# Optimization experiments

Measured on AMD Instinct MI355X. Metric: run time of the kernel, lower is better.

Reference implementation:

```python
import jax, jax.numpy as jnp
import numpy as np

NUM_EXPERTS = 8
TOP_K = 2
AUX_COEF = 0.01
B, S, D, H = 4, 2048, 1024, 684


def setup_inputs() -> dict:
    key = jax.random.key(0)
    ks = jax.random.split(key, 5)
    scale_d = 1.0 / np.sqrt(D)
    scale_h = 1.0 / np.sqrt(H)
    return {
        "x": jax.random.normal(ks[0], (B, S, D), dtype=jnp.float32),
        "router_w": jax.random.normal(ks[1], (NUM_EXPERTS, D), dtype=jnp.float32) * scale_d,
        "w1": jax.random.normal(ks[2], (NUM_EXPERTS, H, D), dtype=jnp.float32) * scale_d,
        "w2": jax.random.normal(ks[3], (NUM_EXPERTS, D, H), dtype=jnp.float32) * scale_h,
        "w3": jax.random.normal(ks[4], (NUM_EXPERTS, H, D), dtype=jnp.float32) * scale_d,
    }


def reference(x, router_w, w1, w2, w3):
    b, s, d = x.shape
    xf = x.reshape(-1, d)                                   # [T, d]
    probs = jax.nn.softmax(xf @ router_w.T, axis=-1)        # [T, E]
    topk_probs, topk_idx = jax.lax.top_k(probs, TOP_K)      # [T, k]

    # aux load-balancing loss (uses top-1 assignment density)
    density = jnp.mean(jax.nn.one_hot(topk_idx[:, 0], NUM_EXPERTS, dtype=xf.dtype), axis=0)
    aux_loss = AUX_COEF * jnp.sum(density * probs.mean(axis=0)) * NUM_EXPERTS

    # per-token per-expert combine weight (sums probs if an expert repeats across slots)
    combine = jnp.sum(jax.nn.one_hot(topk_idx, NUM_EXPERTS, dtype=xf.dtype)
                      * topk_probs[..., None], axis=1)      # [T, E]

    out = jnp.zeros_like(xf)
    for e in range(NUM_EXPERTS):  # fixed small expert loop
        h = jax.nn.silu(xf @ w1[e].T) * (xf @ w3[e].T)      # [T, H] SwiGLU
        out = out + combine[:, e:e + 1] * (h @ w2[e].T)     # weighted scatter-combine
    return out.reshape(b, s, d), aux_loss
```

## Files before the change

kernel.cpp:

```cpp
#include <hip/hip_runtime.h>
#include <hip/hip_bf16.h>

#define T_TOK 8192
#define DMODEL 1024
#define HDIM 684
#define HPAD 704
#define NEXP 8

typedef short  bf16x8  __attribute__((ext_vector_type(8)));
typedef float  f32x4   __attribute__((ext_vector_type(4)));

__device__ inline unsigned short f2bu(float f) {
    __hip_bfloat16 h = __float2bfloat16(f);
    return *reinterpret_cast<unsigned short*>(&h);
}

typedef const __attribute__((address_space(1))) unsigned int* gas_p;
typedef __attribute__((address_space(3))) unsigned int* las_p;
__device__ inline void ld_lds16(const unsigned short* g, unsigned short* l) {
    __builtin_amdgcn_global_load_lds((gas_p)g, (las_p)l, 16, 0, 0);
}


__global__ __launch_bounds__(256) void cvt_bf16x4(
    const float* __restrict__ src, unsigned short* __restrict__ dst, int n4)
{
    int i = blockIdx.x * 256 + threadIdx.x;
    if (i >= n4) return;
    float4 v = ((const float4*)src)[i];
    ushort4 o = make_ushort4(f2bu(v.x), f2bu(v.y), f2bu(v.z), f2bu(v.w));
    ((ushort4*)dst)[i] = o;
}

__global__ __launch_bounds__(256) void cvt_w2_pad(
    const float* __restrict__ w2, unsigned short* __restrict__ w2b, int n)
{
    int i = blockIdx.x * 256 + threadIdx.x;
    if (i >= n) return;
    int row = i / 176;
    int col = (i - row * 176) * 4;
    ushort4 o = make_ushort4(0, 0, 0, 0);
    if (col < HDIM) {
        float4 v = *(const float4*)(w2 + (size_t)row * HDIM + col);
        o = make_ushort4(f2bu(v.x), f2bu(v.y), f2bu(v.z), f2bu(v.w));
    }
    *(ushort4*)(w2b + (size_t)row * HPAD + col) = o;
}

__global__ __launch_bounds__(256) void moe_router(
    const float* __restrict__ x, const float* __restrict__ rw,
    unsigned short* __restrict__ xb,
    float* __restrict__ blk_psum, int* __restrict__ blk_t1, int* __restrict__ blk_pc,
    int* __restrict__ topk_idx, float* __restrict__ topk_p)
{
    __shared__ float sp[4][NEXP];
    __shared__ int   si1[4], si2[4];

    int lane = threadIdx.x & 63;
    int w    = threadIdx.x >> 6;
    int t    = blockIdx.x * 4 + w;
    const float* xr = x + (size_t)t * DMODEL;
    unsigned short* xbr = xb + (size_t)t * DMODEL;

    float acc[NEXP];
#pragma unroll
    for (int e = 0; e < NEXP; ++e) acc[e] = 0.f;
#pragma unroll
    for (int j = 0; j < DMODEL / 64; ++j) {
        float xv = xr[j * 64 + lane];
        xbr[j * 64 + lane] = f2bu(xv);
#pragma unroll
        for (int e = 0; e < NEXP; ++e)
            acc[e] += xv * rw[e * DMODEL + j * 64 + lane];
    }
#pragma unroll
    for (int off = 32; off > 0; off >>= 1) {
#pragma unroll
        for (int e = 0; e < NEXP; ++e)
            acc[e] += __shfl_xor(acc[e], off, 64);
    }
    if (lane == 0) {
        float m = acc[0];
#pragma unroll
        for (int e = 1; e < NEXP; ++e) m = fmaxf(m, acc[e]);
        float p[NEXP]; float s = 0.f;
#pragma unroll
        for (int e = 0; e < NEXP; ++e) { p[e] = expf(acc[e] - m); s += p[e]; }
        float inv = 1.f / s;
#pragma unroll
        for (int e = 0; e < NEXP; ++e) p[e] *= inv;
        int i1 = 0;
#pragma unroll
        for (int e = 1; e < NEXP; ++e) if (p[e] > p[i1]) i1 = e;
        int i2 = (i1 == 0) ? 1 : 0;
#pragma unroll
        for (int e = 0; e < NEXP; ++e) if (e != i1 && p[e] > p[i2]) i2 = e;

        topk_idx[t * 2 + 0] = i1;  topk_idx[t * 2 + 1] = i2;
        topk_p[t * 2 + 0] = p[i1]; topk_p[t * 2 + 1] = p[i2];
#pragma unroll
        for (int e = 0; e < NEXP; ++e) sp[w][e] = p[e];
        si1[w] = i1; si2[w] = i2;
    }
    __syncthreads();
    if (threadIdx.x < NEXP) {
        int e = threadIdx.x;
        float ps = sp[0][e] + sp[1][e] + sp[2][e] + sp[3][e];
        int t1 = (si1[0] == e) + (si1[1] == e) + (si1[2] == e) + (si1[3] == e);
        int pc = t1 + (si2[0] == e) + (si2[1] == e) + (si2[2] == e) + (si2[3] == e);
        blk_psum[blockIdx.x * NEXP + e] = ps;
        blk_t1[blockIdx.x * NEXP + e]  = t1;
        blk_pc[blockIdx.x * NEXP + e]  = pc;
    }
}

__global__ __launch_bounds__(256) void moe_scan(
    const float* __restrict__ blk_psum, const int* __restrict__ blk_t1,
    const int* __restrict__ blk_pc,
    int* pair_count, int* offsets, int* cursor, float* aux_out)
{
    __shared__ float rp[256][NEXP];
    __shared__ int   rt[256][NEXP], rc[256][NEXP];
    __shared__ float tp[NEXP];
    __shared__ int   tt1[NEXP], tpc[NEXP];

    int tid = threadIdx.x;
    float lp[NEXP]; int lt[NEXP], lc[NEXP];
#pragma unroll
    for (int e = 0; e < NEXP; ++e) { lp[e] = 0.f; lt[e] = 0; lc[e] = 0; }
    for (int b = tid; b < 2048; b += 256)
#pragma unroll
        for (int e = 0; e < NEXP; ++e) {
            lp[e] += blk_psum[b * NEXP + e];
            lt[e] += blk_t1[b * NEXP + e];
            lc[e] += blk_pc[b * NEXP + e];
        }
#pragma unroll
    for (int e = 0; e < NEXP; ++e) { rp[tid][e] = lp[e]; rt[tid][e] = lt[e]; rc[tid][e] = lc[e]; }
    __syncthreads();
    if (tid < NEXP) {
        float s = 0.f; int t1 = 0, pc = 0;
        for (int i = 0; i < 256; ++i) { s += rp[i][tid]; t1 += rt[i][tid]; pc += rc[i][tid]; }
        tp[tid] = s; tt1[tid] = t1; tpc[tid] = pc;
        pair_count[tid] = pc;
    }
    __syncthreads();
    if (tid == 0) {
        int run = 0;
        for (int e = 0; e < NEXP; ++e) { offsets[e] = run; cursor[e] = run; run += tpc[e]; }
        float s = 0.f;
        for (int e = 0; e < NEXP; ++e)
            s += ((float)tt1[e] / (float)T_TOK) * (tp[e] / (float)T_TOK);
        aux_out[0] = 0.01f * s * (float)NEXP;
    }
}

__global__ __launch_bounds__(256) void moe_scatter(
    const int* __restrict__ topk_idx, const float* __restrict__ topk_p,
    int* cursor, int* __restrict__ pair_token, float* __restrict__ pair_prob)
{
    __shared__ int lcnt[NEXP], gbase[NEXP];
    int tid = threadIdx.x;
    if (tid < NEXP) lcnt[tid] = 0;
    __syncthreads();
    int t = blockIdx.x * 256 + tid;
    int e0 = topk_idx[t * 2 + 0], e1 = topk_idx[t * 2 + 1];
    int p0 = atomicAdd(&lcnt[e0], 1);
    int p1 = atomicAdd(&lcnt[e1], 1);
    __syncthreads();
    if (tid < NEXP) gbase[tid] = atomicAdd(&cursor[tid], lcnt[tid]);
    __syncthreads();
    int q0 = gbase[e0] + p0, q1 = gbase[e1] + p1;
    pair_token[q0] = t; pair_prob[q0] = topk_p[t * 2 + 0];
    pair_token[q1] = t; pair_prob[q1] = topk_p[t * 2 + 1];
}


__global__ __launch_bounds__(512) void moe_ffn1(
    const unsigned short* __restrict__ xb, const unsigned short* __restrict__ w1b,
    const unsigned short* __restrict__ w3b,
    const int* __restrict__ pair_count, const int* __restrict__ offsets,
    const int* __restrict__ pair_token,
    unsigned short* __restrict__ h)
{
    int e   = blockIdx.z;
    int cnt = pair_count[e];
    int m0  = blockIdx.y * 128;
    if (m0 >= cnt) return;
    int base = offsets[e];
    int n0   = blockIdx.x * 128;

    __shared__ unsigned short aT[4096];
    __shared__ unsigned short b1T[4096];
    __shared__ unsigned short b3T[4096];

    int tid  = threadIdx.x;
    int lane = tid & 63, wave = tid >> 6;
    int wm = wave >> 1, wn = wave & 1;

    int srow = lane >> 2;
    int ksg  = (lane & 3) ^ ((lane >> 3) & 3);
    int arow = m0 + wave * 16 + srow; if (arow >= cnt) arow = cnt - 1;
    const unsigned short* ap  = xb + (size_t)pair_token[base + arow] * DMODEL + ksg * 8;
    int brow = n0 + wave * 16 + srow; if (brow > HDIM - 1) brow = HDIM - 1;
    const unsigned short* b1p = w1b + ((size_t)e * HDIM + brow) * DMODEL + ksg * 8;
    const unsigned short* b3p = w3b + ((size_t)e * HDIM + brow) * DMODEL + ksg * 8;
    unsigned short* lA  = &aT[wave * 512];
    unsigned short* lB1 = &b1T[wave * 512];
    unsigned short* lB3 = &b3T[wave * 512];

    f32x4 acc1[2][4], acc3[2][4];
#pragma unroll
    for (int i = 0; i < 2; ++i)
#pragma unroll
        for (int j = 0; j < 4; ++j) { acc1[i][j] = (f32x4)(0.f); acc3[i][j] = (f32x4)(0.f); }

    int fr  = lane & 15;
    int sz8 = ((lane >> 4) ^ ((fr >> 1) & 3)) * 8;

    for (int k0 = 0; k0 < DMODEL; k0 += 32) {
        ld_lds16(ap + k0, lA);
        ld_lds16(b1p + k0, lB1);
        ld_lds16(b3p + k0, lB3);
        __syncthreads();

        bf16x8 aF[2];
#pragma unroll
        for (int i = 0; i < 2; ++i)
            aF[i] = *(const bf16x8*)&aT[(wm * 32 + i * 16 + fr) * 32 + sz8];
#pragma unroll
        for (int j = 0; j < 4; ++j) {
            int row = (wn * 64 + j * 16 + fr) * 32 + sz8;
            bf16x8 b1F = *(const bf16x8*)&b1T[row];
            bf16x8 b3F = *(const bf16x8*)&b3T[row];
#pragma unroll
            for (int i = 0; i < 2; ++i) {
                acc1[i][j] = __builtin_amdgcn_mfma_f32_16x16x32_bf16(aF[i], b1F, acc1[i][j], 0, 0, 0);
                acc3[i][j] = __builtin_amdgcn_mfma_f32_16x16x32_bf16(aF[i], b3F, acc3[i][j], 0, 0, 0);
            }
        }
        __syncthreads();
    }

    int cbase = n0 + wn * 64 + fr;
    int rbase = m0 + wm * 32 + (lane >> 4) * 4;
#pragma unroll
    for (int i = 0; i < 2; ++i) {
#pragma unroll
        for (int r = 0; r < 4; ++r) {
            int gr = rbase + i * 16 + r;
            if (gr >= cnt) continue;
            unsigned short* hrow = h + (size_t)(base + gr) * HPAD;
#pragma unroll
            for (int j = 0; j < 4; ++j) {
                int col = cbase + j * 16;
                if (col >= HPAD) continue;
                float v1 = acc1[i][j][r];
                float hv = (col < HDIM) ? (v1 / (1.f + expf(-v1))) * acc3[i][j][r] : 0.f;
                hrow[col] = f2bu(hv);
            }
        }
    }
}

__global__ __launch_bounds__(512) void moe_ffn2(
    const unsigned short* __restrict__ h, const unsigned short* __restrict__ w2b,
    const int* __restrict__ pair_count, const int* __restrict__ offsets,
    const int* __restrict__ pair_token, const float* __restrict__ pair_prob,
    float* __restrict__ out)
{
    int e   = blockIdx.z;
    int cnt = pair_count[e];
    int m0  = blockIdx.y * 128;
    if (m0 >= cnt) return;
    int base = offsets[e];
    int n0   = blockIdx.x * 128;

    __shared__ unsigned short aT[4096];
    __shared__ unsigned short bT[4096];

    int tid  = threadIdx.x;
    int lane = tid & 63, wave = tid >> 6;
    int wm = wave >> 1, wn = wave & 1;

    int srow = lane >> 2;
    int ksg  = (lane & 3) ^ ((lane >> 3) & 3);
    int arow = m0 + wave * 16 + srow; if (arow >= cnt) arow = cnt - 1;
    const unsigned short* ap = h + (size_t)(base + arow) * HPAD + ksg * 8;
    const unsigned short* bp = w2b + ((size_t)e * DMODEL + n0 + wave * 16 + srow) * HPAD + ksg * 8;
    unsigned short* lA = &aT[wave * 512];
    unsigned short* lB = &bT[wave * 512];

    f32x4 acc[2][4];
#pragma unroll
    for (int i = 0; i < 2; ++i)
#pragma unroll
        for (int j = 0; j < 4; ++j) acc[i][j] = (f32x4)(0.f);

    int fr  = lane & 15;
    int sz8 = ((lane >> 4) ^ ((fr >> 1) & 3)) * 8;

    for (int k0 = 0; k0 < HPAD; k0 += 32) {
        ld_lds16(ap + k0, lA);
        ld_lds16(bp + k0, lB);
        __syncthreads();

        bf16x8 aF[2];
#pragma unroll
        for (int i = 0; i < 2; ++i)
            aF[i] = *(const bf16x8*)&aT[(wm * 32 + i * 16 + fr) * 32 + sz8];
#pragma unroll
        for (int j = 0; j < 4; ++j) {
            bf16x8 bF = *(const bf16x8*)&bT[(wn * 64 + j * 16 + fr) * 32 + sz8];
#pragma unroll
            for (int i = 0; i < 2; ++i)
                acc[i][j] = __builtin_amdgcn_mfma_f32_16x16x32_bf16(aF[i], bF, acc[i][j], 0, 0, 0);
        }
        __syncthreads();
    }

    int cbase = n0 + wn * 64 + fr;
    int rbase = m0 + wm * 32 + (lane >> 4) * 4;
#pragma unroll
    for (int i = 0; i < 2; ++i) {
#pragma unroll
        for (int r = 0; r < 4; ++r) {
            int gr = rbase + i * 16 + r;
            if (gr >= cnt) continue;
            int gp = base + gr;
            float pw = pair_prob[gp];
            float* orow = out + (size_t)pair_token[gp] * DMODEL;
#pragma unroll
            for (int j = 0; j < 4; ++j)
                atomicAdd(&orow[cbase + j * 16], pw * acc[i][j][r]);
        }
    }
}

extern "C" void kernel_launch(void* const* d_in, const int* in_sizes, int n_in,
                              void* d_out, int out_size, void* d_ws, size_t ws_size,
                              hipStream_t stream)
{
    const float* x  = (const float*)d_in[0];
    const float* rw = (const float*)d_in[1];
    const float* w1 = (const float*)d_in[2];
    const float* w2 = (const float*)d_in[3];
    const float* w3 = (const float*)d_in[4];
    float* out = (float*)d_out;

    char* ws = (char*)d_ws;
    int*   pair_count = (int*)(ws + 0);
    int*   offsets    = (int*)(ws + 32);
    int*   cursor     = (int*)(ws + 64);
    float* blk_psum   = (float*)(ws + 256);
    int*   blk_t1     = (int*)(ws + 65792);
    int*   blk_pc     = (int*)(ws + 131328);
    int*   topk_idx   = (int*)(ws + 196864);
    float* topk_p     = (float*)(ws + 262400);
    int*   pair_token = (int*)(ws + 327936);
    float* pair_prob  = (float*)(ws + 393472);
    unsigned short* xb  = (unsigned short*)(ws + 459264);
    unsigned short* w1b = (unsigned short*)(ws + 17236480);
    unsigned short* w3b = (unsigned short*)(ws + 28443136);
    unsigned short* w2b = (unsigned short*)(ws + 39649792);
    unsigned short* hbuf= (unsigned short*)(ws + 51184128);

    hipMemsetAsync(d_out, 0, (size_t)out_size * sizeof(float), stream);

    cvt_bf16x4<<<(NEXP * HDIM * DMODEL / 4 + 255) / 256, 256, 0, stream>>>(w1, w1b, NEXP * HDIM * DMODEL / 4);
    cvt_bf16x4<<<(NEXP * HDIM * DMODEL / 4 + 255) / 256, 256, 0, stream>>>(w3, w3b, NEXP * HDIM * DMODEL / 4);
    cvt_w2_pad<<<(NEXP * DMODEL * (HPAD / 4) + 255) / 256, 256, 0, stream>>>(w2, w2b, NEXP * DMODEL * (HPAD / 4));

    moe_router <<<T_TOK / 4, 256, 0, stream>>>(x, rw, xb, blk_psum, blk_t1, blk_pc, topk_idx, topk_p);
    moe_scan   <<<1, 256, 0, stream>>>(blk_psum, blk_t1, blk_pc, pair_count, offsets, cursor,
                                       out + (size_t)T_TOK * DMODEL);
    moe_scatter<<<T_TOK / 256, 256, 0, stream>>>(topk_idx, topk_p, cursor, pair_token, pair_prob);

    moe_ffn1<<<dim3(6, 64, 8), 512, 0, stream>>>(xb, w1b, w3b, pair_count, offsets, pair_token, hbuf);
    moe_ffn2<<<dim3(8, 64, 8), 512, 0, stream>>>(hbuf, w2b, pair_count, offsets, pair_token, pair_prob, out);
}
```

Baseline: 333.8 us.

## Double-buffer LDS tiles in both expert GEMMs and merge w1/w3 conversion

Both FFN kernels now use two LDS buffers per operand. The next K-slice's global-to-LDS loads are issued right after the barrier and before the MFMAs on the current slice, and the trailing barrier is removed, leaving one sync per iteration. The aim is to hide global load latency behind matrix math. The w1 and w3 fp32-to-bf16 conversions are merged into one launch to save a kernel launch. The cost is doubled LDS use per block, which is 48KB in ffn1 and may limit occupancy.

```diff
diff --git a/kernel.cpp b/kernel.cpp
--- a/kernel.cpp
+++ b/kernel.cpp
@@ -22,14 +22,18 @@
 }
 
 
-__global__ __launch_bounds__(256) void cvt_bf16x4(
-    const float* __restrict__ src, unsigned short* __restrict__ dst, int n4)
+__global__ __launch_bounds__(256) void cvt_w13(
+    const float* __restrict__ w1, const float* __restrict__ w3,
+    unsigned short* __restrict__ w1b, unsigned short* __restrict__ w3b, int n4)
 {
     int i = blockIdx.x * 256 + threadIdx.x;
-    if (i >= n4) return;
-    float4 v = ((const float4*)src)[i];
+    const float* src; unsigned short* dst; int j;
+    if (i < n4) { src = w1; dst = w1b; j = i; }
+    else if (i < 2 * n4) { src = w3; dst = w3b; j = i - n4; }
+    else return;
+    float4 v = ((const float4*)src)[j];
     ushort4 o = make_ushort4(f2bu(v.x), f2bu(v.y), f2bu(v.z), f2bu(v.w));
-    ((ushort4*)dst)[i] = o;
+    ((ushort4*)dst)[j] = o;
 }
 
 __global__ __launch_bounds__(256) void cvt_w2_pad(
@@ -190,9 +194,9 @@
     int base = offsets[e];
     int n0   = blockIdx.x * 128;
 
-    __shared__ unsigned short aT[4096];
-    __shared__ unsigned short b1T[4096];
-    __shared__ unsigned short b3T[4096];
+    __shared__ unsigned short aT[2][4096];
+    __shared__ unsigned short b1T[2][4096];
+    __shared__ unsigned short b3T[2][4096];
 
     int tid  = threadIdx.x;
     int lane = tid & 63, wave = tid >> 6;
@@ -205,9 +209,9 @@
     int brow = n0 + wave * 16 + srow; if (brow > HDIM - 1) brow = HDIM - 1;
     const unsigned short* b1p = w1b + ((size_t)e * HDIM + brow) * DMODEL + ksg * 8;
     const unsigned short* b3p = w3b + ((size_t)e * HDIM + brow) * DMODEL + ksg * 8;
-    unsigned short* lA  = &aT[wave * 512];
-    unsigned short* lB1 = &b1T[wave * 512];
-    unsigned short* lB3 = &b3T[wave * 512];
+    unsigned short* lA[2]  = { &aT[0][wave * 512],  &aT[1][wave * 512]  };
+    unsigned short* lB1[2] = { &b1T[0][wave * 512], &b1T[1][wave * 512] };
+    unsigned short* lB3[2] = { &b3T[0][wave * 512], &b3T[1][wave * 512] };
 
     f32x4 acc1[2][4], acc3[2][4];
 #pragma unroll
@@ -218,28 +222,39 @@
     int fr  = lane & 15;
     int sz8 = ((lane >> 4) ^ ((fr >> 1) & 3)) * 8;
 
-    for (int k0 = 0; k0 < DMODEL; k0 += 32) {
-        ld_lds16(ap + k0, lA);
-        ld_lds16(b1p + k0, lB1);
-        ld_lds16(b3p + k0, lB3);
+    ld_lds16(ap, lA[0]);
+    ld_lds16(b1p, lB1[0]);
+    ld_lds16(b3p, lB3[0]);
+
+    const int NIT = DMODEL / 32;
+    for (int it = 0; it < NIT; ++it) {
+        int buf = it & 1;
         __syncthreads();
+        if (it + 1 < NIT) {
+            int nk = (it + 1) * 32;
+            ld_lds16(ap + nk,  lA[buf ^ 1]);
+            ld_lds16(b1p + nk, lB1[buf ^ 1]);
+            ld_lds16(b3p + nk, lB3[buf ^ 1]);
+        }
+        const unsigned short* cA  = aT[buf];
+        const unsigned short* cB1 = b1T[buf];
+        const unsigned short* cB3 = b3T[buf];
 
         bf16x8 aF[2];
 #pragma unroll
         for (int i = 0; i < 2; ++i)
-            aF[i] = *(const bf16x8*)&aT[(wm * 32 + i * 16 + fr) * 32 + sz8];
+            aF[i] = *(const bf16x8*)&cA[(wm * 32 + i * 16 + fr) * 32 + sz8];
 #pragma unroll
         for (int j = 0; j < 4; ++j) {
             int row = (wn * 64 + j * 16 + fr) * 32 + sz8;
-            bf16x8 b1F = *(const bf16x8*)&b1T[row];
-            bf16x8 b3F = *(const bf16x8*)&b3T[row];
+            bf16x8 b1F = *(const bf16x8*)&cB1[row];
+            bf16x8 b3F = *(const bf16x8*)&cB3[row];
 #pragma unroll
             for (int i = 0; i < 2; ++i) {
                 acc1[i][j] = __builtin_amdgcn_mfma_f32_16x16x32_bf16(aF[i], b1F, acc1[i][j], 0, 0, 0);
                 acc3[i][j] = __builtin_amdgcn_mfma_f32_16x16x32_bf16(aF[i], b3F, acc3[i][j], 0, 0, 0);
             }
         }
-        __syncthreads();
     }
 
     int cbase = n0 + wn * 64 + fr;
@@ -276,8 +291,8 @@
     int base = offsets[e];
     int n0   = blockIdx.x * 128;
 
-    __shared__ unsigned short aT[4096];
-    __shared__ unsigned short bT[4096];
+    __shared__ unsigned short aT[2][4096];
+    __shared__ unsigned short bT[2][4096];
 
     int tid  = threadIdx.x;
     int lane = tid & 63, wave = tid >> 6;
@@ -288,8 +303,8 @@
     int arow = m0 + wave * 16 + srow; if (arow >= cnt) arow = cnt - 1;
     const unsigned short* ap = h + (size_t)(base + arow) * HPAD + ksg * 8;
     const unsigned short* bp = w2b + ((size_t)e * DMODEL + n0 + wave * 16 + srow) * HPAD + ksg * 8;
-    unsigned short* lA = &aT[wave * 512];
-    unsigned short* lB = &bT[wave * 512];
+    unsigned short* lA[2] = { &aT[0][wave * 512], &aT[1][wave * 512] };
+    unsigned short* lB[2] = { &bT[0][wave * 512], &bT[1][wave * 512] };
 
     f32x4 acc[2][4];
 #pragma unroll
@@ -300,23 +315,32 @@
     int fr  = lane & 15;
     int sz8 = ((lane >> 4) ^ ((fr >> 1) & 3)) * 8;
 
-    for (int k0 = 0; k0 < HPAD; k0 += 32) {
-        ld_lds16(ap + k0, lA);
-        ld_lds16(bp + k0, lB);
+    ld_lds16(ap, lA[0]);
+    ld_lds16(bp, lB[0]);
+
+    const int NIT = HPAD / 32;
+    for (int it = 0; it < NIT; ++it) {
+        int buf = it & 1;
         __syncthreads();
+        if (it + 1 < NIT) {
+            int nk = (it + 1) * 32;
+            ld_lds16(ap + nk, lA[buf ^ 1]);
+            ld_lds16(bp + nk, lB[buf ^ 1]);
+        }
+        const unsigned short* cA = aT[buf];
+        const unsigned short* cB = bT[buf];
 
         bf16x8 aF[2];
 #pragma unroll
         for (int i = 0; i < 2; ++i)
-            aF[i] = *(const bf16x8*)&aT[(wm * 32 + i * 16 + fr) * 32 + sz8];
+            aF[i] = *(const bf16x8*)&cA[(wm * 32 + i * 16 + fr) * 32 + sz8];
 #pragma unroll
         for (int j = 0; j < 4; ++j) {
-            bf16x8 bF = *(const bf16x8*)&bT[(wn * 64 + j * 16 + fr) * 32 + sz8];
+            bf16x8 bF = *(const bf16x8*)&cB[(wn * 64 + j * 16 + fr) * 32 + sz8];
 #pragma unroll
             for (int i = 0; i < 2; ++i)
                 acc[i][j] = __builtin_amdgcn_mfma_f32_16x16x32_bf16(aF[i], bF, acc[i][j], 0, 0, 0);
         }
-        __syncthreads();
     }
 
     int cbase = n0 + wn * 64 + fr;
@@ -367,8 +391,8 @@
 
     hipMemsetAsync(d_out, 0, (size_t)out_size * sizeof(float), stream);
 
-    cvt_bf16x4<<<(NEXP * HDIM * DMODEL / 4 + 255) / 256, 256, 0, stream>>>(w1, w1b, NEXP * HDIM * DMODEL / 4);
-    cvt_bf16x4<<<(NEXP * HDIM * DMODEL / 4 + 255) / 256, 256, 0, stream>>>(w3, w3b, NEXP * HDIM * DMODEL / 4);
+    int n4 = NEXP * HDIM * DMODEL / 4;
+    cvt_w13<<<(2 * n4 + 255) / 256, 256, 0, stream>>>(w1, w3, w1b, w3b, n4);
     cvt_w2_pad<<<(NEXP * DMODEL * (HPAD / 4) + 255) / 256, 256, 0, stream>>>(w2, w2b, NEXP * DMODEL * (HPAD / 4));
 
     moe_router <<<T_TOK / 4, 256, 0, stream>>>(x, rw, xb, blk_psum, blk_t1, blk_pc, topk_idx, topk_p);
```

After: 326.4 us. 1.02x faster.
